# Optimization experiments

Measured on AMD Instinct MI355X. Metric: run time of the kernel, lower is better.

The kernel has to match this reference:

```python
import jax, jax.numpy as jnp
import numpy as np

DIM = 4096
HEADS = 32
HEAD_DIM = 128
FFN_INNER = 4 * DIM  # GEGLU inner
EPS = 1e-6


def _mk(key, shape, scale=0.02):
    return jax.random.normal(key, shape, dtype=jnp.float32) * scale


def setup_inputs() -> dict:
    key = jax.random.key(0)
    ks = jax.random.split(key, 20)
    inp = {
        "video": jax.random.normal(ks[0], (1, 4096, DIM), dtype=jnp.float32),
        "text": jax.random.normal(ks[1], (1, 256, DIM), dtype=jnp.float32),
        # self-attention projections
        "wq": _mk(ks[2], (DIM, DIM)),
        "wk": _mk(ks[3], (DIM, DIM)),
        "wv": _mk(ks[4], (DIM, DIM)),
        "wo": _mk(ks[5], (DIM, DIM)),
        "q_norm_w": jnp.ones((DIM,), jnp.float32),
        "k_norm_w": jnp.ones((DIM,), jnp.float32),
        # cross-attention projections (q from video, k/v from text)
        "cwq": _mk(ks[6], (DIM, DIM)),
        "cwk": _mk(ks[7], (DIM, DIM)),
        "cwv": _mk(ks[8], (DIM, DIM)),
        "cwo": _mk(ks[9], (DIM, DIM)),
        "cq_norm_w": jnp.ones((DIM,), jnp.float32),
        "ck_norm_w": jnp.ones((DIM,), jnp.float32),
        # GEGLU FFN: proj -> (value, gate) -> value * gelu(gate) -> down
        "w_ff_proj": _mk(ks[10], (DIM, 2 * FFN_INNER)),
        "w_ff_down": _mk(ks[11], (FFN_INNER, DIM)),
    }
    return inp


def rmsnorm(x, w, eps=EPS):
    # RMSNorm over full hidden dim in fp32 (matches DistributedRMSNorm global math)
    x32 = x.astype(jnp.float32)
    rms = jax.lax.rsqrt(jnp.mean(x32 * x32, axis=-1, keepdims=True) + eps)
    return (x32 * rms) * w


def split_heads(x):  # [b,s,dim] -> [b,h,s,hd]
    b, s, _ = x.shape
    return x.reshape(b, s, HEADS, HEAD_DIM).transpose(0, 2, 1, 3)


def merge_heads(x):  # [b,h,s,hd] -> [b,s,dim]
    b, h, s, hd = x.shape
    return x.transpose(0, 2, 1, 3).reshape(b, s, h * hd)


def bmm_sdpa(q, k, v):
    # BMM + softmax fallback (explicit score matrix, as on Neuron)
    scale = 1.0 / np.sqrt(HEAD_DIM)
    scores = jnp.einsum("bhqd,bhkd->bhqk", q, k) * scale
    probs = jax.nn.softmax(scores, axis=-1)
    return jnp.einsum("bhqk,bhkd->bhqd", probs, v)


def attention(x_q, x_kv, wq, wk, wv, wo, qn, kn):
    q = rmsnorm(x_q @ wq, qn)
    k = rmsnorm(x_kv @ wk, kn)
    v = x_kv @ wv
    out = bmm_sdpa(split_heads(q), split_heads(k), split_heads(v))
    return merge_heads(out) @ wo


def geglu_ffn(x, w_proj, w_down):
    h = x @ w_proj
    val, gate = jnp.split(h, 2, axis=-1)
    return (val * jax.nn.gelu(gate)) @ w_down


def reference(video, text, wq, wk, wv, wo, q_norm_w, k_norm_w,
              cwq, cwk, cwv, cwo, cq_norm_w, ck_norm_w,
              w_ff_proj, w_ff_down):
    # video self-attention block slice
    h = video + attention(video, video, wq, wk, wv, wo, q_norm_w, k_norm_w)
    # text cross-attention
    h = h + attention(h, text, cwq, cwk, cwv, cwo, cq_norm_w, ck_norm_w)
    # GEGLU feed-forward
    h = h + geglu_ffn(h, w_ff_proj, w_ff_down)
    return h
```

## Files before the change

### kernel.cpp

```cpp
#include <hip/hip_runtime.h>
#include <cstdint>
#include <cstddef>

typedef __bf16 bf16;
typedef __bf16 bf16x8 __attribute__((ext_vector_type(8)));
typedef __bf16 bf16x4 __attribute__((ext_vector_type(4)));
typedef float f32x4 __attribute__((ext_vector_type(4)));

static constexpr int D = 4096;
static constexpr int S = 4096;
static constexpr int T = 256;
static constexpr int H = 32;
static constexpr int F = 16384;

__device__ __forceinline__ void gload16(const void* g, void* l) {
  __builtin_amdgcn_global_load_lds((const __attribute__((address_space(1))) void*)g,
                                   (__attribute__((address_space(3))) void*)l, 16, 0, 0);
}

#define MFMA16(a, b, c) __builtin_amdgcn_mfma_f32_16x16x32_bf16((a), (b), (c), 0, 0, 0)

__global__ __launch_bounds__(256) void k_cvt(const float* __restrict__ in, bf16* __restrict__ out, int n) {
  int i = (blockIdx.x * 256 + threadIdx.x) * 4;
  if (i >= n) return;
  float4 v = *(const float4*)(in + i);
  bf16x4 o = { (bf16)v.x, (bf16)v.y, (bf16)v.z, (bf16)v.w };
  *(bf16x4*)(out + i) = o;
}

__global__ __launch_bounds__(256) void k_tc(const float* __restrict__ in, bf16* __restrict__ out,
                                            int R, int C, int ldin) {
  __shared__ float tile[64][65];
  const int c0 = blockIdx.x * 64, r0 = blockIdx.y * 64;
  const int x = threadIdx.x, y = threadIdx.y;
  #pragma unroll
  for (int i = 0; i < 16; i++) {
    const int yy = y + 4 * i;
    tile[yy][x] = in[(size_t)(r0 + yy) * ldin + c0 + x];
  }
  __syncthreads();
  #pragma unroll
  for (int i = 0; i < 16; i++) {
    const int yy = y + 4 * i;
    out[(size_t)(c0 + yy) * R + r0 + x] = (bf16)tile[x][yy];
  }
}

__global__ __launch_bounds__(256) void k_tb(const bf16* __restrict__ in, bf16* __restrict__ out,
                                            int R, int C, int ldin) {
  __shared__ bf16 tile[32][33];
  int c0 = blockIdx.x * 32, r0 = blockIdx.y * 32;
  int x = threadIdx.x, y = threadIdx.y;
  #pragma unroll
  for (int yy = y; yy < 32; yy += 8)
    tile[yy][x] = in[(size_t)(r0 + yy) * ldin + c0 + x];
  __syncthreads();
  #pragma unroll
  for (int yy = y; yy < 32; yy += 8)
    out[(size_t)(c0 + yy) * R + r0 + x] = tile[x][yy];
}

__global__ __launch_bounds__(256) void k_rms(const bf16* __restrict__ in, const float* __restrict__ w,
                                             bf16* __restrict__ out, int ldin, float sc) {
  const int row = blockIdx.x, t = threadIdx.x;
  const bf16* x = in + (size_t)row * ldin;
  float xv[16];
  float ss = 0.f;
  #pragma unroll
  for (int i = 0; i < 2; i++) {
    bf16x8 b = *(const bf16x8*)(x + t * 8 + i * 2048);
    #pragma unroll
    for (int j = 0; j < 8; j++) { xv[i * 8 + j] = (float)b[j]; ss += xv[i * 8 + j] * xv[i * 8 + j]; }
  }
  #pragma unroll
  for (int off = 1; off < 64; off <<= 1) ss += __shfl_xor(ss, off, 64);
  __shared__ float red[4];
  if ((t & 63) == 0) red[t >> 6] = ss;
  __syncthreads();
  float rms = rsqrtf((red[0] + red[1] + red[2] + red[3]) * (1.f / 4096.f) + 1e-6f) * sc;
  #pragma unroll
  for (int i = 0; i < 2; i++) {
    float4 w0 = *(const float4*)(w + t * 8 + i * 2048);
    float4 w1 = *(const float4*)(w + t * 8 + i * 2048 + 4);
    bf16x8 ov;
    ov[0] = (bf16)(xv[i * 8 + 0] * rms * w0.x); ov[1] = (bf16)(xv[i * 8 + 1] * rms * w0.y);
    ov[2] = (bf16)(xv[i * 8 + 2] * rms * w0.z); ov[3] = (bf16)(xv[i * 8 + 3] * rms * w0.w);
    ov[4] = (bf16)(xv[i * 8 + 4] * rms * w1.x); ov[5] = (bf16)(xv[i * 8 + 5] * rms * w1.y);
    ov[6] = (bf16)(xv[i * 8 + 6] * rms * w1.z); ov[7] = (bf16)(xv[i * 8 + 7] * rms * w1.w);
    *(bf16x8*)(out + (size_t)row * 4096 + t * 8 + i * 2048) = ov;
  }
}

__device__ __forceinline__ void xcd_map(int orig, int XGM, int BYG, int BXG, int& by, int& bx) {
  const int xcd = orig & 7, oidx = orig >> 3;
  by = (xcd % XGM) * BYG + oidx % BYG;
  bx = (xcd / XGM) * BXG + oidx / BYG;
}

template <int MODE>
__global__ __launch_bounds__(512, 2) void k_gemm2(const bf16* __restrict__ A, const bf16* __restrict__ BT,
                                                  float* __restrict__ Cf, bf16* __restrict__ Cb,
                                                  const float* __restrict__ res,
                                                  int M, int N, int K, int XGM, int BYG, int BXG) {
  __shared__ bf16 LA[2][2][256 * 32];
  __shared__ bf16 LB[2][2][256 * 32];
  int by, bx;
  xcd_map(blockIdx.x, XGM, BYG, BXG, by, bx);
  const size_t m0 = (size_t)by * 256, n0 = (size_t)bx * 256;
  const int t = threadIdx.x;
  const int w = t >> 6, lane = t & 63;
  const int wm = w >> 2, wn = w & 3;
  const int g = lane >> 4, r15 = lane & 15;
  const int nt = K >> 6;
  const int sr0 = t >> 2, ss0 = t & 3;
  const int sr1 = (t + 512) >> 2, ss1 = (t + 512) & 3;
  const int sc0 = ((ss0 ^ ((sr0 >> 1) & 3)) << 3);
  const int sc1 = ((ss1 ^ ((sr1 >> 1) & 3)) << 3);
  f32x4 acc[8][4] = {};

  auto stA = [&](int db, int kh, int st) {
    const bf16* src = A + m0 * K + (size_t)st * 64 + kh * 32;
    gload16(src + (size_t)sr0 * K + sc0, &LA[db][kh][t * 8]);
    gload16(src + (size_t)sr1 * K + sc1, &LA[db][kh][(t + 512) * 8]);
  };
  auto stB = [&](int db, int kh, int st) {
    const bf16* src = BT + n0 * K + (size_t)st * 64 + kh * 32;
    gload16(src + (size_t)sr0 * K + sc0, &LB[db][kh][t * 8]);
    gload16(src + (size_t)sr1 * K + sc1, &LB[db][kh][(t + 512) * 8]);
  };

  stA(0, 0, 0); stB(0, 0, 0); stA(0, 1, 0); stB(0, 1, 0);
  stA(1, 0, 1); stB(1, 0, 1); stA(1, 1, 1);
  asm volatile("s_waitcnt vmcnt(10)" ::: "memory");
  __builtin_amdgcn_s_barrier();

  const int arow = wm * 128;

#define GEMM_TILE(DD, TC)                                                                     \
  {                                                                                           \
    const int t1 = ((TC) + 1 < nt) ? (TC) + 1 : nt - 1;                                       \
    const int t2 = ((TC) + 2 < nt) ? (TC) + 2 : nt - 1;                                       \
    bf16x8 af[8], b0, b1;                                                                     \
    stB((DD) ^ 1, 1, t1);                                                                     \
    _Pragma("unroll")                                                                         \
    for (int mf = 0; mf < 8; ++mf) {                                                          \
      const int rr = arow + mf * 16 + r15;                                                    \
      af[mf] = *(const bf16x8*)&LA[DD][0][rr * 32 + ((g ^ ((rr >> 1) & 3)) << 3)];            \
    }                                                                                         \
    {                                                                                         \
      const int rb0 = wn * 64 + r15, rb1 = wn * 64 + 16 + r15;                                \
      b0 = *(const bf16x8*)&LB[DD][0][rb0 * 32 + ((g ^ ((rb0 >> 1) & 3)) << 3)];              \
      b1 = *(const bf16x8*)&LB[DD][0][rb1 * 32 + ((g ^ ((rb1 >> 1) & 3)) << 3)];              \
    }                                                                                         \
    __builtin_amdgcn_s_barrier();                                                             \
    __builtin_amdgcn_s_setprio(1);                                                            \
    _Pragma("unroll")                                                                         \
    for (int mf = 0; mf < 8; ++mf) {                                                          \
      acc[mf][0] = MFMA16(af[mf], b0, acc[mf][0]);                                            \
      acc[mf][1] = MFMA16(af[mf], b1, acc[mf][1]);                                            \
    }                                                                                         \
    __builtin_amdgcn_s_setprio(0);                                                            \
    stA(DD, 0, t2);                                                                           \
    {                                                                                         \
      const int rb0 = wn * 64 + 32 + r15, rb1 = wn * 64 + 48 + r15;                           \
      b0 = *(const bf16x8*)&LB[DD][0][rb0 * 32 + ((g ^ ((rb0 >> 1) & 3)) << 3)];              \
      b1 = *(const bf16x8*)&LB[DD][0][rb1 * 32 + ((g ^ ((rb1 >> 1) & 3)) << 3)];              \
    }                                                                                         \
    asm volatile("s_waitcnt vmcnt(10)" ::: "memory");                                         \
    __builtin_amdgcn_s_barrier();                                                             \
    __builtin_amdgcn_s_setprio(1);                                                            \
    _Pragma("unroll")                                                                         \
    for (int mf = 0; mf < 8; ++mf) {                                                          \
      acc[mf][2] = MFMA16(af[mf], b0, acc[mf][2]);                                            \
      acc[mf][3] = MFMA16(af[mf], b1, acc[mf][3]);                                            \
    }                                                                                         \
    __builtin_amdgcn_s_setprio(0);                                                            \
    stB(DD, 0, t2);                                                                           \
    _Pragma("unroll")                                                                         \
    for (int mf = 0; mf < 8; ++mf) {                                                          \
      const int rr = arow + mf * 16 + r15;                                                    \
      af[mf] = *(const bf16x8*)&LA[DD][1][rr * 32 + ((g ^ ((rr >> 1) & 3)) << 3)];            \
    }                                                                                         \
    {                                                                                         \
      const int rb0 = wn * 64 + r15, rb1 = wn * 64 + 16 + r15;                                \
      b0 = *(const bf16x8*)&LB[DD][1][rb0 * 32 + ((g ^ ((rb0 >> 1) & 3)) << 3)];              \
      b1 = *(const bf16x8*)&LB[DD][1][rb1 * 32 + ((g ^ ((rb1 >> 1) & 3)) << 3)];              \
    }                                                                                         \
    __builtin_amdgcn_s_barrier();                                                             \
    __builtin_amdgcn_s_setprio(1);                                                            \
    _Pragma("unroll")                                                                         \
    for (int mf = 0; mf < 8; ++mf) {                                                          \
      acc[mf][0] = MFMA16(af[mf], b0, acc[mf][0]);                                            \
      acc[mf][1] = MFMA16(af[mf], b1, acc[mf][1]);                                            \
    }                                                                                         \
    __builtin_amdgcn_s_setprio(0);                                                            \
    stA(DD, 1, t2);                                                                           \
    {                                                                                         \
      const int rb0 = wn * 64 + 32 + r15, rb1 = wn * 64 + 48 + r15;                           \
      b0 = *(const bf16x8*)&LB[DD][1][rb0 * 32 + ((g ^ ((rb0 >> 1) & 3)) << 3)];              \
      b1 = *(const bf16x8*)&LB[DD][1][rb1 * 32 + ((g ^ ((rb1 >> 1) & 3)) << 3)];              \
    }                                                                                         \
    asm volatile("s_waitcnt vmcnt(10)" ::: "memory");                                         \
    __builtin_amdgcn_s_barrier();                                                             \
    __builtin_amdgcn_s_setprio(1);                                                            \
    _Pragma("unroll")                                                                         \
    for (int mf = 0; mf < 8; ++mf) {                                                          \
      acc[mf][2] = MFMA16(af[mf], b0, acc[mf][2]);                                            \
      acc[mf][3] = MFMA16(af[mf], b1, acc[mf][3]);                                            \
    }                                                                                         \
    __builtin_amdgcn_s_setprio(0);                                                            \
  }

  for (int tt = 0; tt < nt; tt += 2) {
    GEMM_TILE(0, tt);
    GEMM_TILE(1, tt + 1);
  }
#undef GEMM_TILE

  #pragma unroll
  for (int mf = 0; mf < 8; ++mf)
    #pragma unroll
    for (int nf = 0; nf < 4; ++nf) {
      const size_t col = n0 + wn * 64 + nf * 16 + r15;
      #pragma unroll
      for (int rr = 0; rr < 4; ++rr) {
        const size_t row = m0 + wm * 128 + mf * 16 + g * 4 + rr;
        const size_t idx = row * (size_t)N + col;
        const float v = acc[mf][nf][rr];
        if (MODE == 0) Cf[idx] = v;
        else if (MODE == 1) Cb[idx] = (bf16)v;
        else if (MODE == 2) Cf[idx] = v + res[idx];
        else { const float s = v + res[idx]; Cf[idx] = s; Cb[idx] = (bf16)s; }
      }
    }
}

__global__ __launch_bounds__(512, 2) void k_geglu2(const bf16* __restrict__ A, const bf16* __restrict__ BT,
                                                   bf16* __restrict__ G, int N, int K,
                                                   int XGM, int BYG, int BXG) {
  __shared__ bf16 LA[2][2][256 * 32];
  __shared__ bf16 LBv[2][2][128 * 32];
  __shared__ bf16 LBg[2][2][128 * 32];
  int by, bx;
  xcd_map(blockIdx.x, XGM, BYG, BXG, by, bx);
  const size_t m0 = (size_t)by * 256, n0 = (size_t)bx * 128;
  const int t = threadIdx.x;
  const int w = t >> 6, lane = t & 63;
  const int wm = w >> 2, wn = w & 3;
  const int g = lane >> 4, r15 = lane & 15;
  const int nt = K >> 6;
  const int sr0 = t >> 2, ss0 = t & 3;
  const int sr1 = (t + 512) >> 2, ss1 = (t + 512) & 3;
  const int sc0 = ((ss0 ^ ((sr0 >> 1) & 3)) << 3);
  const int sc1 = ((ss1 ^ ((sr1 >> 1) & 3)) << 3);
  f32x4 av[8][2] = {}, ag[8][2] = {};

  auto stA = [&](int db, int kh, int st) {
    const bf16* src = A + m0 * K + (size_t)st * 64 + kh * 32;
    gload16(src + (size_t)sr0 * K + sc0, &LA[db][kh][t * 8]);
    gload16(src + (size_t)sr1 * K + sc1, &LA[db][kh][(t + 512) * 8]);
  };
  auto stBv = [&](int db, int kh, int st) {
    const bf16* src = BT + n0 * K + (size_t)st * 64 + kh * 32;
    gload16(src + (size_t)sr0 * K + sc0, &LBv[db][kh][t * 8]);
  };
  auto stBg = [&](int db, int kh, int st) {
    const bf16* src = BT + ((size_t)N + n0) * K + (size_t)st * 64 + kh * 32;
    gload16(src + (size_t)sr0 * K + sc0, &LBg[db][kh][t * 8]);
  };

  stA(0, 0, 0); stBv(0, 0, 0); stBg(0, 0, 0); stA(0, 1, 0); stBv(0, 1, 0); stBg(0, 1, 0);
  stA(1, 0, 1); stBv(1, 0, 1); stBg(1, 0, 1); stA(1, 1, 1);
  asm volatile("s_waitcnt vmcnt(10)" ::: "memory");
  __builtin_amdgcn_s_barrier();

  const int arow = wm * 128;

#define GEGLU_TILE(DD, TC)                                                                    \
  {                                                                                           \
    const int t1 = ((TC) + 1 < nt) ? (TC) + 1 : nt - 1;                                       \
    const int t2 = ((TC) + 2 < nt) ? (TC) + 2 : nt - 1;                                       \
    bf16x8 af[8], b0, b1;                                                                     \
    stBv((DD) ^ 1, 1, t1); stBg((DD) ^ 1, 1, t1);                                             \
    _Pragma("unroll")                                                                         \
    for (int mf = 0; mf < 8; ++mf) {                                                          \
      const int rr = arow + mf * 16 + r15;                                                    \
      af[mf] = *(const bf16x8*)&LA[DD][0][rr * 32 + ((g ^ ((rr >> 1) & 3)) << 3)];            \
    }                                                                                         \
    {                                                                                         \
      const int rb0 = wn * 32 + r15, rb1 = wn * 32 + 16 + r15;                                \
      b0 = *(const bf16x8*)&LBv[DD][0][rb0 * 32 + ((g ^ ((rb0 >> 1) & 3)) << 3)];             \
      b1 = *(const bf16x8*)&LBv[DD][0][rb1 * 32 + ((g ^ ((rb1 >> 1) & 3)) << 3)];             \
    }                                                                                         \
    __builtin_amdgcn_s_barrier();                                                             \
    __builtin_amdgcn_s_setprio(1);                                                            \
    _Pragma("unroll")                                                                         \
    for (int mf = 0; mf < 8; ++mf) {                                                          \
      av[mf][0] = MFMA16(af[mf], b0, av[mf][0]);                                              \
      av[mf][1] = MFMA16(af[mf], b1, av[mf][1]);                                              \
    }                                                                                         \
    __builtin_amdgcn_s_setprio(0);                                                            \
    stA(DD, 0, t2);                                                                           \
    {                                                                                         \
      const int rb0 = wn * 32 + r15, rb1 = wn * 32 + 16 + r15;                                \
      b0 = *(const bf16x8*)&LBg[DD][0][rb0 * 32 + ((g ^ ((rb0 >> 1) & 3)) << 3)];             \
      b1 = *(const bf16x8*)&LBg[DD][0][rb1 * 32 + ((g ^ ((rb1 >> 1) & 3)) << 3)];             \
    }                                                                                         \
    asm volatile("s_waitcnt vmcnt(10)" ::: "memory");                                         \
    __builtin_amdgcn_s_barrier();                                                             \
    __builtin_amdgcn_s_setprio(1);                                                            \
    _Pragma("unroll")                                                                         \
    for (int mf = 0; mf < 8; ++mf) {                                                          \
      ag[mf][0] = MFMA16(af[mf], b0, ag[mf][0]);                                              \
      ag[mf][1] = MFMA16(af[mf], b1, ag[mf][1]);                                              \
    }                                                                                         \
    __builtin_amdgcn_s_setprio(0);                                                            \
    stBv(DD, 0, t2); stBg(DD, 0, t2);                                                         \
    _Pragma("unroll")                                                                         \
    for (int mf = 0; mf < 8; ++mf) {                                                          \
      const int rr = arow + mf * 16 + r15;                                                    \
      af[mf] = *(const bf16x8*)&LA[DD][1][rr * 32 + ((g ^ ((rr >> 1) & 3)) << 3)];            \
    }                                                                                         \
    {                                                                                         \
      const int rb0 = wn * 32 + r15, rb1 = wn * 32 + 16 + r15;                                \
      b0 = *(const bf16x8*)&LBv[DD][1][rb0 * 32 + ((g ^ ((rb0 >> 1) & 3)) << 3)];             \
      b1 = *(const bf16x8*)&LBv[DD][1][rb1 * 32 + ((g ^ ((rb1 >> 1) & 3)) << 3)];             \
    }                                                                                         \
    __builtin_amdgcn_s_barrier();                                                             \
    __builtin_amdgcn_s_setprio(1);                                                            \
    _Pragma("unroll")                                                                         \
    for (int mf = 0; mf < 8; ++mf) {                                                          \
      av[mf][0] = MFMA16(af[mf], b0, av[mf][0]);                                              \
      av[mf][1] = MFMA16(af[mf], b1, av[mf][1]);                                              \
    }                                                                                         \
    __builtin_amdgcn_s_setprio(0);                                                            \
    stA(DD, 1, t2);                                                                           \
    {                                                                                         \
      const int rb0 = wn * 32 + r15, rb1 = wn * 32 + 16 + r15;                                \
      b0 = *(const bf16x8*)&LBg[DD][1][rb0 * 32 + ((g ^ ((rb0 >> 1) & 3)) << 3)];             \
      b1 = *(const bf16x8*)&LBg[DD][1][rb1 * 32 + ((g ^ ((rb1 >> 1) & 3)) << 3)];             \
    }                                                                                         \
    asm volatile("s_waitcnt vmcnt(10)" ::: "memory");                                         \
    __builtin_amdgcn_s_barrier();                                                             \
    __builtin_amdgcn_s_setprio(1);                                                            \
    _Pragma("unroll")                                                                         \
    for (int mf = 0; mf < 8; ++mf) {                                                          \
      ag[mf][0] = MFMA16(af[mf], b0, ag[mf][0]);                                              \
      ag[mf][1] = MFMA16(af[mf], b1, ag[mf][1]);                                              \
    }                                                                                         \
    __builtin_amdgcn_s_setprio(0);                                                            \
  }

  for (int tt = 0; tt < nt; tt += 2) {
    GEGLU_TILE(0, tt);
    GEGLU_TILE(1, tt + 1);
  }
#undef GEGLU_TILE

  #pragma unroll
  for (int mf = 0; mf < 8; ++mf)
    #pragma unroll
    for (int nf = 0; nf < 2; ++nf) {
      const size_t col = n0 + wn * 32 + nf * 16 + r15;
      #pragma unroll
      for (int rr = 0; rr < 4; ++rr) {
        const size_t row = m0 + wm * 128 + mf * 16 + g * 4 + rr;
        const float val = av[mf][nf][rr], gt = ag[mf][nf][rr];
        const float z = 1.595769122f * gt + 0.0713548162f * gt * gt * gt;
        const float gel = gt / (1.f + __expf(-z));
        G[row * (size_t)N + col] = (bf16)(val * gel);
      }
    }
}

template <int MODE>
__global__ __launch_bounds__(256) void k_gemm128(const bf16* __restrict__ A, const bf16* __restrict__ BT,
                                                 float* __restrict__ Cf, bf16* __restrict__ Cb,
                                                 int M, int N, int K) {
  __shared__ bf16 As[128 * 32];
  __shared__ bf16 Bs[128 * 32];
  const int t = threadIdx.x;
  const int lane = t & 63, w = t >> 6;
  const int wr = w >> 1, wc = w & 1;
  const int g = lane >> 4, r15 = lane & 15;
  const size_t m0 = (size_t)blockIdx.y * 128, n0 = (size_t)blockIdx.x * 128;
  f32x4 acc[4][4] = {};
  const int c0 = t, c1 = t + 256;
  const int ar0 = c0 >> 2, as0 = c0 & 3, ar1 = c1 >> 2, as1 = c1 & 3;
  const bf16* Ab = A + m0 * K;
  const bf16* Bb = BT + n0 * K;
  for (int k0 = 0; k0 < K; k0 += 32) {
    __syncthreads();
    gload16(Ab + (size_t)ar0 * K + k0 + ((as0 ^ (ar0 & 3)) << 3), &As[c0 * 8]);
    gload16(Ab + (size_t)ar1 * K + k0 + ((as1 ^ (ar1 & 3)) << 3), &As[c1 * 8]);
    gload16(Bb + (size_t)ar0 * K + k0 + ((as0 ^ (ar0 & 3)) << 3), &Bs[c0 * 8]);
    gload16(Bb + (size_t)ar1 * K + k0 + ((as1 ^ (ar1 & 3)) << 3), &Bs[c1 * 8]);
    __syncthreads();
    bf16x8 af[4], bfr[4];
    #pragma unroll
    for (int mi = 0; mi < 4; mi++) {
      int row = wr * 64 + mi * 16 + r15;
      af[mi] = *(const bf16x8*)&As[row * 32 + ((g ^ (row & 3)) << 3)];
    }
    #pragma unroll
    for (int ni = 0; ni < 4; ni++) {
      int row = wc * 64 + ni * 16 + r15;
      bfr[ni] = *(const bf16x8*)&Bs[row * 32 + ((g ^ (row & 3)) << 3)];
    }
    #pragma unroll
    for (int mi = 0; mi < 4; mi++)
      #pragma unroll
      for (int ni = 0; ni < 4; ni++)
        acc[mi][ni] = MFMA16(af[mi], bfr[ni], acc[mi][ni]);
  }
  #pragma unroll
  for (int mi = 0; mi < 4; mi++)
    #pragma unroll
    for (int ni = 0; ni < 4; ni++) {
      size_t col = n0 + wc * 64 + ni * 16 + r15;
      #pragma unroll
      for (int rr = 0; rr < 4; rr++) {
        size_t row = m0 + wr * 64 + mi * 16 + g * 4 + rr;
        size_t idx = row * (size_t)N + col;
        float v = acc[mi][ni][rr];
        if (MODE == 0) Cf[idx] = v;
        else Cb[idx] = (bf16)v;
      }
    }
}

__global__ __launch_bounds__(256) void k_attn(const bf16* __restrict__ Q, const bf16* __restrict__ Kb,
                                              const bf16* __restrict__ VT, bf16* __restrict__ O,
                                              int Skv) {
  __shared__ bf16 Kt[64 * 128];
  __shared__ bf16 Vt[128 * 64];
  __shared__ bf16 Pt[4][16 * 64];
  const int h = blockIdx.y;
  const int t = threadIdx.x, w = t >> 6, lane = t & 63;
  const int g = lane >> 4, r15 = lane & 15;
  const int q0 = blockIdx.x * 64 + w * 16;
  bf16x8 qf[4];
  #pragma unroll
  for (int c = 0; c < 4; c++)
    qf[c] = *(const bf16x8*)(Q + (size_t)(q0 + r15) * D + h * 128 + c * 32 + g * 8);
  f32x4 o[8] = {};
  float m_[4] = { -1e30f, -1e30f, -1e30f, -1e30f };
  float l_[4] = { 0.f, 0.f, 0.f, 0.f };
  for (int kt = 0; kt < Skv; kt += 64) {
    __syncthreads();
    #pragma unroll
    for (int cc = 0; cc < 4; cc++) {
      int c = t + cc * 256;
      int kr = c >> 4, ks = c & 15;
      gload16(Kb + (size_t)(kt + kr) * D + h * 128 + ((ks ^ (kr & 15)) << 3), &Kt[c * 8]);
      int vr = c >> 3, vs = c & 7;
      gload16(VT + (size_t)(h * 128 + vr) * Skv + kt + ((vs ^ (vr & 7)) << 3), &Vt[c * 8]);
    }
    __syncthreads();
    f32x4 s[4] = {};
    __builtin_amdgcn_s_setprio(1);
    #pragma unroll
    for (int c = 0; c < 4; c++) {
      #pragma unroll
      for (int j = 0; j < 4; j++) {
        const int row = j * 16 + r15;
        bf16x8 kf = *(const bf16x8*)&Kt[row * 128 + (((4 * c + g) ^ (row & 15)) << 3)];
        s[j] = MFMA16(qf[c], kf, s[j]);
      }
    }
    __builtin_amdgcn_s_setprio(0);
    float sv[4][4], mxs[4];
    bool grow = false;
    #pragma unroll
    for (int rr = 0; rr < 4; rr++) {
      sv[rr][0] = s[0][rr]; sv[rr][1] = s[1][rr]; sv[rr][2] = s[2][rr]; sv[rr][3] = s[3][rr];
      float mx = fmaxf(fmaxf(sv[rr][0], sv[rr][1]), fmaxf(sv[rr][2], sv[rr][3]));
      #pragma unroll
      for (int off = 1; off < 16; off <<= 1) mx = fmaxf(mx, __shfl_xor(mx, off, 16));
      mxs[rr] = mx;
      grow = grow || (mx > m_[rr]);
    }
    if (__any(grow ? 1 : 0)) {
      float al[4];
      #pragma unroll
      for (int rr = 0; rr < 4; rr++) {
        float mn = fmaxf(m_[rr], mxs[rr]);
        al[rr] = __expf(m_[rr] - mn);
        l_[rr] *= al[rr];
        m_[rr] = mn;
      }
      #pragma unroll
      for (int d = 0; d < 8; d++)
        #pragma unroll
        for (int rr = 0; rr < 4; rr++) o[d][rr] *= al[rr];
    }
    #pragma unroll
    for (int rr = 0; rr < 4; rr++) {
      float p0 = __expf(sv[rr][0] - m_[rr]), p1 = __expf(sv[rr][1] - m_[rr]);
      float p2 = __expf(sv[rr][2] - m_[rr]), p3 = __expf(sv[rr][3] - m_[rr]);
      float sm = p0 + p1 + p2 + p3;
      #pragma unroll
      for (int off = 1; off < 16; off <<= 1) sm += __shfl_xor(sm, off, 16);
      l_[rr] += sm;
      const int prow = g * 4 + rr;
      const int sbase = prow * 64, sx = prow & 7, e = r15 & 7, hi = r15 >> 3;
      Pt[w][sbase + (((0 + hi) ^ sx) << 3) + e] = (bf16)p0;
      Pt[w][sbase + (((2 + hi) ^ sx) << 3) + e] = (bf16)p1;
      Pt[w][sbase + (((4 + hi) ^ sx) << 3) + e] = (bf16)p2;
      Pt[w][sbase + (((6 + hi) ^ sx) << 3) + e] = (bf16)p3;
    }
    bf16x8 pa[2];
    #pragma unroll
    for (int kk = 0; kk < 2; kk++)
      pa[kk] = *(const bf16x8*)&Pt[w][r15 * 64 + (((kk * 4 + g) ^ (r15 & 7)) << 3)];
    __builtin_amdgcn_s_setprio(1);
    #pragma unroll
    for (int d = 0; d < 8; d++) {
      const int vrow = d * 16 + r15;
      #pragma unroll
      for (int kk = 0; kk < 2; kk++) {
        bf16x8 vbf = *(const bf16x8*)&Vt[vrow * 64 + (((kk * 4 + g) ^ (vrow & 7)) << 3)];
        o[d] = MFMA16(pa[kk], vbf, o[d]);
      }
    }
    __builtin_amdgcn_s_setprio(0);
  }
  #pragma unroll
  for (int rr = 0; rr < 4; rr++) {
    float inv = 1.f / l_[rr];
    #pragma unroll
    for (int d = 0; d < 8; d++)
      O[(size_t)(q0 + g * 4 + rr) * D + h * 128 + d * 16 + r15] = (bf16)(o[d][rr] * inv);
  }
}

extern "C" void kernel_launch(void* const* d_in, const int* in_sizes, int n_in,
                              void* d_out, int out_size, void* d_ws, size_t ws_size,
                              hipStream_t stream) {
  (void)in_sizes; (void)n_in; (void)out_size; (void)ws_size;
  const float* video = (const float*)d_in[0];
  const float* text  = (const float*)d_in[1];
  const float* wq    = (const float*)d_in[2];
  const float* wk    = (const float*)d_in[3];
  const float* wv    = (const float*)d_in[4];
  const float* wo    = (const float*)d_in[5];
  const float* qnw   = (const float*)d_in[6];
  const float* knw   = (const float*)d_in[7];
  const float* cwq   = (const float*)d_in[8];
  const float* cwk   = (const float*)d_in[9];
  const float* cwv   = (const float*)d_in[10];
  const float* cwo   = (const float*)d_in[11];
  const float* cqnw  = (const float*)d_in[12];
  const float* cknw  = (const float*)d_in[13];
  const float* ffp   = (const float*)d_in[14];
  const float* ffd   = (const float*)d_in[15];
  float* out = (float*)d_out;
  const float SCQ = 0.08838834764831845f;

  char* slab = (char*)d_ws;
  const size_t MB = 1024 * 1024;
  bf16*  wbuf   = (bf16*)slab;
  bf16*  vt     = (bf16*)(slab + 96 * MB);
  bf16*  preqkv = (bf16*)(slab + 128 * MB);
  bf16*  Hval   = (bf16*)(slab + 268 * MB);
  char* p = slab + 402 * MB;
  auto take = [&](size_t bytes) { char* r = p; p += (bytes + 255) & ~(size_t)255; return r; };
  bf16* xb   = (bf16*)take((size_t)S * D * 2);
  bf16* qb   = (bf16*)take((size_t)S * D * 2);
  bf16* kb   = (bf16*)take((size_t)S * D * 2);
  bf16* ab   = (bf16*)take((size_t)S * D * 2);
  float* h1  = (float*)take((size_t)S * D * 4);
  bf16* tbuf = (bf16*)take((size_t)T * D * 2);
  bf16* ckb  = (bf16*)take((size_t)T * D * 2);
  bf16* cvb  = (bf16*)take((size_t)T * D * 2);
  bf16* cvt_ = (bf16*)take((size_t)T * D * 2);
  float* h2  = out;

  dim3 b256(256), b512(512), btc(64, 4), btb(32, 8);
  const int GRID_DD = 256, GRID_GG = 2048, GRID_QKV = 768;

  k_cvt<<<(S * D) / 1024, b256, 0, stream>>>(video, xb, S * D);
  k_tc<<<dim3(D / 64, D / 64), btc, 0, stream>>>(wq, wbuf, D, D, D);
  k_tc<<<dim3(D / 64, D / 64), btc, 0, stream>>>(wk, wbuf + (size_t)D * D, D, D, D);
  k_tc<<<dim3(D / 64, D / 64), btc, 0, stream>>>(wv, wbuf + 2 * (size_t)D * D, D, D, D);
  k_gemm2<1><<<GRID_QKV, b512, 0, stream>>>(xb, wbuf, nullptr, preqkv, nullptr, S, 3 * D, D, 2, 8, 12);
  k_rms<<<S, b256, 0, stream>>>(preqkv, qnw, qb, 3 * D, SCQ);
  k_rms<<<S, b256, 0, stream>>>(preqkv + D, knw, kb, 3 * D, 1.f);
  k_tb<<<dim3(D / 32, S / 32), btb, 0, stream>>>(preqkv + 2 * D, vt, S, D, 3 * D);
  k_attn<<<dim3(S / 64, H), b256, 0, stream>>>(qb, kb, vt, ab, S);
  k_tc<<<dim3(D / 64, D / 64), btc, 0, stream>>>(wo, wbuf, D, D, D);
  k_gemm2<3><<<GRID_DD, b512, 0, stream>>>(ab, wbuf, h1, xb, video, S, D, D, 2, 8, 4);

  k_tc<<<dim3(D / 64, D / 64), btc, 0, stream>>>(cwq, wbuf, D, D, D);
  k_gemm2<1><<<GRID_DD, b512, 0, stream>>>(xb, wbuf, nullptr, preqkv, nullptr, S, D, D, 2, 8, 4);
  k_rms<<<S, b256, 0, stream>>>(preqkv, cqnw, qb, D, SCQ);
  k_cvt<<<(T * D) / 1024, b256, 0, stream>>>(text, tbuf, T * D);
  k_tc<<<dim3(D / 64, D / 64), btc, 0, stream>>>(cwk, wbuf, D, D, D);
  k_gemm128<1><<<dim3(D / 128, T / 128), b256, 0, stream>>>(tbuf, wbuf, nullptr, preqkv, T, D, D);
  k_rms<<<T, b256, 0, stream>>>(preqkv, cknw, ckb, D, 1.f);
  k_tc<<<dim3(D / 64, D / 64), btc, 0, stream>>>(cwv, wbuf, D, D, D);
  k_gemm128<1><<<dim3(D / 128, T / 128), b256, 0, stream>>>(tbuf, wbuf, nullptr, cvb, T, D, D);
  k_tb<<<dim3(D / 32, T / 32), btb, 0, stream>>>(cvb, cvt_, T, D, D);
  k_attn<<<dim3(S / 64, H), b256, 0, stream>>>(qb, ckb, cvt_, ab, T);
  k_tc<<<dim3(D / 64, D / 64), btc, 0, stream>>>(cwo, wbuf, D, D, D);
  k_gemm2<3><<<GRID_DD, b512, 0, stream>>>(ab, wbuf, h2, xb, h1, S, D, D, 2, 8, 4);

  k_tc<<<dim3((2 * F) / 64, D / 64), btc, 0, stream>>>(ffp, wbuf, D, 2 * F, 2 * F);
  k_geglu2<<<GRID_GG, b512, 0, stream>>>(xb, wbuf, Hval, F, D, 2, 8, 32);
  k_tc<<<dim3(D / 64, F / 64), btc, 0, stream>>>(ffd, wbuf, F, D, D);
  k_gemm2<2><<<GRID_DD, b512, 0, stream>>>(Hval, wbuf, out, nullptr, h2, S, D, F, 2, 8, 4);
}
```

Baseline: 3.654 ms.

## Batch weight transposes, fuse QK RMSNorms and cross KV GEMMs, prefetch A fragments

Three separate fp32-to-bf16 weight transposes become one launch through a z-indexed kernel. The q and k RMSNorm launches are merged into one two-row-group kernel. The cross-attention K and V projections now run as a single GEMM over a concatenated weight, which removes one launch and an intermediate buffer. In the gemm2 and GEGLU inner loops, the second half-K A fragments are loaded into a separate register array right after the barrier, so LDS reads overlap the preceding MFMAs, at the cost of higher register pressure.

Measured after the change: 3.551 ms. 1.03x faster.

```diff
diff --git a/kernel.cpp b/kernel.cpp
--- a/kernel.cpp
+++ b/kernel.cpp
@@ -43,6 +43,27 @@
   for (int i = 0; i < 16; i++) {
     const int yy = y + 4 * i;
     out[(size_t)(c0 + yy) * R + r0 + x] = (bf16)tile[x][yy];
+  }
+}
+
+__global__ __launch_bounds__(256) void k_tc3(const float* __restrict__ s0, const float* __restrict__ s1,
+                                             const float* __restrict__ s2, bf16* __restrict__ d0,
+                                             bf16* __restrict__ d1, bf16* __restrict__ d2) {
+  const float* in = blockIdx.z == 0 ? s0 : (blockIdx.z == 1 ? s1 : s2);
+  bf16* out = blockIdx.z == 0 ? d0 : (blockIdx.z == 1 ? d1 : d2);
+  __shared__ float tile[64][65];
+  const int c0 = blockIdx.x * 64, r0 = blockIdx.y * 64;
+  const int x = threadIdx.x, y = threadIdx.y;
+  #pragma unroll
+  for (int i = 0; i < 16; i++) {
+    const int yy = y + 4 * i;
+    tile[yy][x] = in[(size_t)(r0 + yy) * D + c0 + x];
+  }
+  __syncthreads();
+  #pragma unroll
+  for (int i = 0; i < 16; i++) {
+    const int yy = y + 4 * i;
+    out[(size_t)(c0 + yy) * D + r0 + x] = (bf16)tile[x][yy];
   }
 }
 
@@ -87,6 +108,42 @@
     ov[2] = (bf16)(xv[i * 8 + 2] * rms * w0.z); ov[3] = (bf16)(xv[i * 8 + 3] * rms * w0.w);
     ov[4] = (bf16)(xv[i * 8 + 4] * rms * w1.x); ov[5] = (bf16)(xv[i * 8 + 5] * rms * w1.y);
     ov[6] = (bf16)(xv[i * 8 + 6] * rms * w1.z); ov[7] = (bf16)(xv[i * 8 + 7] * rms * w1.w);
+    *(bf16x8*)(out + (size_t)row * 4096 + t * 8 + i * 2048) = ov;
+  }
+}
+
+__global__ __launch_bounds__(256) void k_rms2(const bf16* __restrict__ in, const float* __restrict__ w0,
+                                              const float* __restrict__ w1, bf16* __restrict__ out0,
+                                              bf16* __restrict__ out1, int ldin, float sc0) {
+  const int which = blockIdx.y;
+  const float* w = which ? w1 : w0;
+  bf16* out = which ? out1 : out0;
+  const float sc = which ? 1.f : sc0;
+  const int row = blockIdx.x, t = threadIdx.x;
+  const bf16* x = in + (size_t)row * ldin + which * D;
+  float xv[16];
+  float ss = 0.f;
+  #pragma unroll
+  for (int i = 0; i < 2; i++) {
+    bf16x8 b = *(const bf16x8*)(x + t * 8 + i * 2048);
+    #pragma unroll
+    for (int j = 0; j < 8; j++) { xv[i * 8 + j] = (float)b[j]; ss += xv[i * 8 + j] * xv[i * 8 + j]; }
+  }
+  #pragma unroll
+  for (int off = 1; off < 64; off <<= 1) ss += __shfl_xor(ss, off, 64);
+  __shared__ float red[4];
+  if ((t & 63) == 0) red[t >> 6] = ss;
+  __syncthreads();
+  float rms = rsqrtf((red[0] + red[1] + red[2] + red[3]) * (1.f / 4096.f) + 1e-6f) * sc;
+  #pragma unroll
+  for (int i = 0; i < 2; i++) {
+    float4 v0 = *(const float4*)(w + t * 8 + i * 2048);
+    float4 v1 = *(const float4*)(w + t * 8 + i * 2048 + 4);
+    bf16x8 ov;
+    ov[0] = (bf16)(xv[i * 8 + 0] * rms * v0.x); ov[1] = (bf16)(xv[i * 8 + 1] * rms * v0.y);
+    ov[2] = (bf16)(xv[i * 8 + 2] * rms * v0.z); ov[3] = (bf16)(xv[i * 8 + 3] * rms * v0.w);
+    ov[4] = (bf16)(xv[i * 8 + 4] * rms * v1.x); ov[5] = (bf16)(xv[i * 8 + 5] * rms * v1.y);
+    ov[6] = (bf16)(xv[i * 8 + 6] * rms * v1.z); ov[7] = (bf16)(xv[i * 8 + 7] * rms * v1.w);
     *(bf16x8*)(out + (size_t)row * 4096 + t * 8 + i * 2048) = ov;
   }
 }
@@ -140,7 +197,8 @@
   {                                                                                           \
     const int t1 = ((TC) + 1 < nt) ? (TC) + 1 : nt - 1;                                       \
     const int t2 = ((TC) + 2 < nt) ? (TC) + 2 : nt - 1;                                       \
-    bf16x8 af[8], b0, b1;                                                                     \
+    bf16x8 af[8], af2[8], b0, b1;                                                             \
+                                                                     \
     stB((DD) ^ 1, 1, t1);                                                                     \
     _Pragma("unroll")                                                                         \
     for (int mf = 0; mf < 8; ++mf) {                                                          \
@@ -160,6 +218,7 @@
       acc[mf][1] = MFMA16(af[mf], b1, acc[mf][1]);                                            \
     }                                                                                         \
     __builtin_amdgcn_s_setprio(0);                                                            \
+                 \
     stA(DD, 0, t2);                                                                           \
     {                                                                                         \
       const int rb0 = wn * 64 + 32 + r15, rb1 = wn * 64 + 48 + r15;                           \
@@ -168,6 +227,11 @@
     }                                                                                         \
     asm volatile("s_waitcnt vmcnt(10)" ::: "memory");                                         \
     __builtin_amdgcn_s_barrier();                                                             \
+    _Pragma("unroll")                                                                         \
+    for (int mf = 0; mf < 8; ++mf) {                                                          \
+      const int rr = arow + mf * 16 + r15;                                                    \
+      af2[mf] = *(const bf16x8*)&LA[DD][1][rr * 32 + ((g ^ ((rr >> 1) & 3)) << 3)];           \
+    }                                                                                         \
     __builtin_amdgcn_s_setprio(1);                                                            \
     _Pragma("unroll")                                                                         \
     for (int mf = 0; mf < 8; ++mf) {                                                          \
@@ -175,12 +239,8 @@
       acc[mf][3] = MFMA16(af[mf], b1, acc[mf][3]);                                            \
     }                                                                                         \
     __builtin_amdgcn_s_setprio(0);                                                            \
+                                               \
     stB(DD, 0, t2);                                                                           \
-    _Pragma("unroll")                                                                         \
-    for (int mf = 0; mf < 8; ++mf) {                                                          \
-      const int rr = arow + mf * 16 + r15;                                                    \
-      af[mf] = *(const bf16x8*)&LA[DD][1][rr * 32 + ((g ^ ((rr >> 1) & 3)) << 3)];            \
-    }                                                                                         \
     {                                                                                         \
       const int rb0 = wn * 64 + r15, rb1 = wn * 64 + 16 + r15;                                \
       b0 = *(const bf16x8*)&LB[DD][1][rb0 * 32 + ((g ^ ((rb0 >> 1) & 3)) << 3)];              \
@@ -190,10 +250,11 @@
     __builtin_amdgcn_s_setprio(1);                                                            \
     _Pragma("unroll")                                                                         \
     for (int mf = 0; mf < 8; ++mf) {                                                          \
-      acc[mf][0] = MFMA16(af[mf], b0, acc[mf][0]);                                            \
-      acc[mf][1] = MFMA16(af[mf], b1, acc[mf][1]);                                            \
-    }                                                                                         \
-    __builtin_amdgcn_s_setprio(0);                                                            \
+      acc[mf][0] = MFMA16(af2[mf], b0, acc[mf][0]);                                           \
+      acc[mf][1] = MFMA16(af2[mf], b1, acc[mf][1]);                                           \
+    }                                                                                         \
+    __builtin_amdgcn_s_setprio(0);                                                            \
+                                                                     \
     stA(DD, 1, t2);                                                                           \
     {                                                                                         \
       const int rb0 = wn * 64 + 32 + r15, rb1 = wn * 64 + 48 + r15;                           \
@@ -205,8 +266,8 @@
     __builtin_amdgcn_s_setprio(1);                                                            \
     _Pragma("unroll")                                                                         \
     for (int mf = 0; mf < 8; ++mf) {                                                          \
-      acc[mf][2] = MFMA16(af[mf], b0, acc[mf][2]);                                            \
-      acc[mf][3] = MFMA16(af[mf], b1, acc[mf][3]);                                            \
+      acc[mf][2] = MFMA16(af2[mf], b0, acc[mf][2]);                                           \
+      acc[mf][3] = MFMA16(af2[mf], b1, acc[mf][3]);                                           \
     }                                                                                         \
     __builtin_amdgcn_s_setprio(0);                                                            \
   }
@@ -280,7 +341,8 @@
   {                                                                                           \
     const int t1 = ((TC) + 1 < nt) ? (TC) + 1 : nt - 1;                                       \
     const int t2 = ((TC) + 2 < nt) ? (TC) + 2 : nt - 1;                                       \
-    bf16x8 af[8], b0, b1;                                                                     \
+    bf16x8 af[8], af2[8], b0, b1;                                                             \
+                                                                       \
     stBv((DD) ^ 1, 1, t1); stBg((DD) ^ 1, 1, t1);                                             \
     _Pragma("unroll")                                                                         \
     for (int mf = 0; mf < 8; ++mf) {                                                          \
@@ -300,6 +362,7 @@
       av[mf][1] = MFMA16(af[mf], b1, av[mf][1]);                                              \
     }                                                                                         \
     __builtin_amdgcn_s_setprio(0);                                                            \
+                                               \
     stA(DD, 0, t2);                                                                           \
     {                                                                                         \
       const int rb0 = wn * 32 + r15, rb1 = wn * 32 + 16 + r15;                                \
@@ -308,6 +371,11 @@
     }                                                                                         \
     asm volatile("s_waitcnt vmcnt(10)" ::: "memory");                                         \
     __builtin_amdgcn_s_barrier();                                                             \
+    _Pragma("unroll")                                                                         \
+    for (int mf = 0; mf < 8; ++mf) {                                                          \
+      const int rr = arow + mf * 16 + r15;                                                    \
+      af2[mf] = *(const bf16x8*)&LA[DD][1][rr * 32 + ((g ^ ((rr >> 1) & 3)) << 3)];           \
+    }                                                                                         \
     __builtin_amdgcn_s_setprio(1);                                                            \
     _Pragma("unroll")                                                                         \
     for (int mf = 0; mf < 8; ++mf) {                                                          \
@@ -315,12 +383,8 @@
       ag[mf][1] = MFMA16(af[mf], b1, ag[mf][1]);                                              \
     }                                                                                         \
     __builtin_amdgcn_s_setprio(0);                                                            \
+                                                           \
     stBv(DD, 0, t2); stBg(DD, 0, t2);                                                         \
-    _Pragma("unroll")                                                                         \
-    for (int mf = 0; mf < 8; ++mf) {                                                          \
-      const int rr = arow + mf * 16 + r15;                                                    \
-      af[mf] = *(const bf16x8*)&LA[DD][1][rr * 32 + ((g ^ ((rr >> 1) & 3)) << 3)];            \
-    }                                                                                         \
     {                                                                                         \
       const int rb0 = wn * 32 + r15, rb1 = wn * 32 + 16 + r15;                                \
       b0 = *(const bf16x8*)&LBv[DD][1][rb0 * 32 + ((g ^ ((rb0 >> 1) & 3)) << 3)];             \
@@ -330,10 +394,11 @@
     __builtin_amdgcn_s_setprio(1);                                                            \
     _Pragma("unroll")                                                                         \
     for (int mf = 0; mf < 8; ++mf) {                                                          \
-      av[mf][0] = MFMA16(af[mf], b0, av[mf][0]);                                              \
-      av[mf][1] = MFMA16(af[mf], b1, av[mf][1]);                                              \
-    }                                                                                         \
-    __builtin_amdgcn_s_setprio(0);                                                            \
+      av[mf][0] = MFMA16(af2[mf], b0, av[mf][0]);                                             \
+      av[mf][1] = MFMA16(af2[mf], b1, av[mf][1]);                                             \
+    }                                                                                         \
+    __builtin_amdgcn_s_setprio(0);                                                            \
+                                                                      \
     stA(DD, 1, t2);                                                                           \
     {                                                                                         \
       const int rb0 = wn * 32 + r15, rb1 = wn * 32 + 16 + r15;                                \
@@ -345,8 +410,8 @@
     __builtin_amdgcn_s_setprio(1);                                                            \
     _Pragma("unroll")                                                                         \
     for (int mf = 0; mf < 8; ++mf) {                                                          \
-      ag[mf][0] = MFMA16(af[mf], b0, ag[mf][0]);                                              \
-      ag[mf][1] = MFMA16(af[mf], b1, ag[mf][1]);                                              \
+      ag[mf][0] = MFMA16(af2[mf], b0, ag[mf][0]);                                             \
+      ag[mf][1] = MFMA16(af2[mf], b1, ag[mf][1]);                                             \
     }                                                                                         \
     __builtin_amdgcn_s_setprio(0);                                                            \
   }
@@ -572,7 +637,6 @@
   float* h1  = (float*)take((size_t)S * D * 4);
   bf16* tbuf = (bf16*)take((size_t)T * D * 2);
   bf16* ckb  = (bf16*)take((size_t)T * D * 2);
-  bf16* cvb  = (bf16*)take((size_t)T * D * 2);
   bf16* cvt_ = (bf16*)take((size_t)T * D * 2);
   float* h2  = out;
 
@@ -580,12 +644,10 @@
   const int GRID_DD = 256, GRID_GG = 2048, GRID_QKV = 768;
 
   k_cvt<<<(S * D) / 1024, b256, 0, stream>>>(video, xb, S * D);
-  k_tc<<<dim3(D / 64, D / 64), btc, 0, stream>>>(wq, wbuf, D, D, D);
-  k_tc<<<dim3(D / 64, D / 64), btc, 0, stream>>>(wk, wbuf + (size_t)D * D, D, D, D);
-  k_tc<<<dim3(D / 64, D / 64), btc, 0, stream>>>(wv, wbuf + 2 * (size_t)D * D, D, D, D);
+  k_tc3<<<dim3(D / 64, D / 64, 3), btc, 0, stream>>>(wq, wk, wv, wbuf, wbuf + (size_t)D * D,
+                                                     wbuf + 2 * (size_t)D * D);
   k_gemm2<1><<<GRID_QKV, b512, 0, stream>>>(xb, wbuf, nullptr, preqkv, nullptr, S, 3 * D, D, 2, 8, 12);
-  k_rms<<<S, b256, 0, stream>>>(preqkv, qnw, qb, 3 * D, SCQ);
-  k_rms<<<S, b256, 0, stream>>>(preqkv + D, knw, kb, 3 * D, 1.f);
+  k_rms2<<<dim3(S, 2), b256, 0, stream>>>(preqkv, qnw, knw, qb, kb, 3 * D, SCQ);
   k_tb<<<dim3(D / 32, S / 32), btb, 0, stream>>>(preqkv + 2 * D, vt, S, D, 3 * D);
   k_attn<<<dim3(S / 64, H), b256, 0, stream>>>(qb, kb, vt, ab, S);
   k_tc<<<dim3(D / 64, D / 64), btc, 0, stream>>>(wo, wbuf, D, D, D);
@@ -595,12 +657,11 @@
   k_gemm2<1><<<GRID_DD, b512, 0, stream>>>(xb, wbuf, nullptr, preqkv, nullptr, S, D, D, 2, 8, 4);
   k_rms<<<S, b256, 0, stream>>>(preqkv, cqnw, qb, D, SCQ);
   k_cvt<<<(T * D) / 1024, b256, 0, stream>>>(text, tbuf, T * D);
-  k_tc<<<dim3(D / 64, D / 64), btc, 0, stream>>>(cwk, wbuf, D, D, D);
-  k_gemm128<1><<<dim3(D / 128, T / 128), b256, 0, stream>>>(tbuf, wbuf, nullptr, preqkv, T, D, D);
-  k_rms<<<T, b256, 0, stream>>>(preqkv, cknw, ckb, D, 1.f);
-  k_tc<<<dim3(D / 64, D / 64), btc, 0, stream>>>(cwv, wbuf, D, D, D);
-  k_gemm128<1><<<dim3(D / 128, T / 128), b256, 0, stream>>>(tbuf, wbuf, nullptr, cvb, T, D, D);
-  k_tb<<<dim3(D / 32, T / 32), btb, 0, stream>>>(cvb, cvt_, T, D, D);
+  k_tc3<<<dim3(D / 64, D / 64, 2), btc, 0, stream>>>(cwk, cwv, cwv, wbuf, wbuf + (size_t)D * D,
+                                                     wbuf + (size_t)D * D);
+  k_gemm128<1><<<dim3((2 * D) / 128, T / 128), b256, 0, stream>>>(tbuf, wbuf, nullptr, preqkv, T, 2 * D, D);
+  k_rms<<<T, b256, 0, stream>>>(preqkv, cknw, ckb, 2 * D, 1.f);
+  k_tb<<<dim3(D / 32, T / 32), btb, 0, stream>>>(preqkv + D, cvt_, T, D, 2 * D);
   k_attn<<<dim3(S / 64, H), b256, 0, stream>>>(qb, ckb, cvt_, ab, T);
   k_tc<<<dim3(D / 64, D / 64), btc, 0, stream>>>(cwo, wbuf, D, D, D);
   k_gemm2<3><<<GRID_DD, b512, 0, stream>>>(ab, wbuf, h2, xb, h1, S, D, D, 2, 8, 4);
```
